# Performance work log

Hardware: AMD Instinct MI355X
Metric: run time of the kernel (lower is better)

The kernel has to match this reference:

```python
import jax, jax.numpy as jnp
import numpy as np

B, S, E, H = 2, 2048, 1024, 16
D = E // H


def setup_inputs() -> dict:
    key = jax.random.key(0)
    ks = jax.random.split(key, 7)
    return {
        "query": jax.random.normal(ks[0], (B, S, E), dtype=jnp.float32),
        "key": jax.random.normal(ks[1], (B, S, E), dtype=jnp.float32),
        "value": jax.random.normal(ks[2], (B, S, E), dtype=jnp.float32),
        "Wq": jax.random.normal(ks[3], (E, E), dtype=jnp.float32) * (E ** -0.5),
        "Wk": jax.random.normal(ks[4], (E, E), dtype=jnp.float32) * (E ** -0.5),
        "Wv": jax.random.normal(ks[5], (E, E), dtype=jnp.float32) * (E ** -0.5),
        "Wo": jax.random.normal(ks[6], (E, E), dtype=jnp.float32) * (E ** -0.5),
    }


def reference(query, key, value, Wq, Wk, Wv, Wo):
    emb_dim = query.shape[-1]
    h = H
    d = emb_dim // h
    # QuantLinear with all-None quantizers == plain Linear (no bias):
    # torch Linear computes x @ W.T with W of shape [out, in].
    q = query @ Wq.T   # [b, s, e]
    k = key @ Wk.T
    v = value @ Wv.T
    # b s (h d) -> b h s d
    def split_heads(x):
        b, s, e = x.shape
        return x.reshape(b, s, h, d).transpose(0, 2, 1, 3)
    q = split_heads(q)
    k = split_heads(k)
    v = split_heads(v)
    # NOTE: faithful to source — scale uses full emb_dim, not head_dim.
    scale = emb_dim ** (-0.5)
    scores = jnp.einsum('bhsd,bhtd->bhst', q * scale, k)  # [b,h,s,s]
    weights = jax.nn.softmax(scores, axis=-1)  # QuantIdentity(None) == identity; dropout p=0
    heads = jnp.einsum('bhst,bhtd->bhsd', weights, v)
    # b h s d -> b s (h d)
    b = heads.shape[0]
    out = heads.transpose(0, 2, 1, 3).reshape(b, -1, emb_dim)
    return out @ Wo.T
```

## Files before the change

kernel.cpp:

```cpp
#include <hip/hip_runtime.h>
#include <hip/hip_bf16.h>
#include <stdint.h>

typedef __attribute__((ext_vector_type(8))) short s16x8;
typedef __attribute__((ext_vector_type(4))) float f32x4;
typedef __attribute__((ext_vector_type(16))) float f32x16;

#define QSCALE 0.045084220027780106f

__device__ __forceinline__ unsigned short f2bf(float f) {
    union { float f; uint32_t u; } v; v.f = f;
    uint32_t u = v.u;
    u += 0x7FFFu + ((u >> 16) & 1u);
    return (unsigned short)(u >> 16);
}

__device__ __forceinline__ unsigned int pkbf2(float a, float b) {
    union { __hip_bfloat162 h; unsigned int u; } x;
    x.h = __float22bfloat162_rn(float2{a, b});
    return x.u;
}

#define GLOAD_LDS16(gptr, lptr)                                                         \
    __builtin_amdgcn_global_load_lds(                                                   \
        (const __attribute__((address_space(1))) unsigned int*)(gptr),                  \
        (__attribute__((address_space(3))) unsigned int*)(lptr), 16, 0, 0)

__global__ __launch_bounds__(256)
void cvt_all(const float* __restrict__ q, const float* __restrict__ k,
             const float* __restrict__ v, const float* __restrict__ wq,
             const float* __restrict__ wk, const float* __restrict__ wv,
             const float* __restrict__ wo,
             unsigned short* __restrict__ xq, unsigned short* __restrict__ xk,
             unsigned short* __restrict__ xv, unsigned short* __restrict__ wqb,
             unsigned short* __restrict__ wkb, unsigned short* __restrict__ wvb,
             unsigned short* __restrict__ wob)
{
    int bid = blockIdx.x;
    const float* src; unsigned short* dst; int rel;
    if (bid < 6144) {
        int s = bid >> 11; rel = bid & 2047;
        src = (s == 0) ? q : (s == 1) ? k : v;
        dst = (s == 0) ? xq : (s == 1) ? xk : xv;
    } else {
        int s = (bid - 6144) >> 9; rel = (bid - 6144) & 511;
        src = (s == 0) ? wq : (s == 1) ? wk : (s == 2) ? wv : wo;
        dst = (s == 0) ? wqb : (s == 1) ? wkb : (s == 2) ? wvb : wob;
    }
    size_t i = (size_t)rel * 256 + threadIdx.x;
    const float4* p = (const float4*)src;
    float4 a = p[i * 2];
    float4 b2 = p[i * 2 + 1];
    s16x8 r;
    r[0] = (short)f2bf(a.x);  r[1] = (short)f2bf(a.y);
    r[2] = (short)f2bf(a.z);  r[3] = (short)f2bf(a.w);
    r[4] = (short)f2bf(b2.x); r[5] = (short)f2bf(b2.y);
    r[6] = (short)f2bf(b2.z); r[7] = (short)f2bf(b2.w);
    *(s16x8*)(dst + i * 8) = r;
}

__device__ __forceinline__ void gemm_tile512(const unsigned short* __restrict__ A,
                                             const unsigned short* __restrict__ Bt,
                                             void* __restrict__ C,
                                             int N, int K, int f32out, float cscale,
                                             unsigned short* Al, unsigned short* Bl)
{
    const int tid  = threadIdx.x;
    const int lane = tid & 63;
    const int w    = tid >> 6;
    const int wr   = w >> 2, wc = w & 3;
    const int l15  = lane & 15, l4 = lane >> 4;

    const int m0 = blockIdx.x * 128;
    const int n0 = blockIdx.y * 128;

    f32x4 acc[4][2];
#pragma unroll
    for (int i = 0; i < 4; ++i)
#pragma unroll
        for (int j = 0; j < 2; ++j) acc[i][j] = (f32x4){0.f, 0.f, 0.f, 0.f};

    const int slin = w * 64 + lane;
    const int srow = slin >> 2;
    const int scol = ((slin & 3) ^ ((srow >> 1) & 3)) * 8;

    int aoff[4], boff[2];
#pragma unroll
    for (int mi = 0; mi < 4; ++mi) {
        int rowa = wr * 64 + mi * 16 + l15;
        aoff[mi] = rowa * 32 + ((l4 ^ ((rowa >> 1) & 3)) * 8);
    }
#pragma unroll
    for (int nf = 0; nf < 2; ++nf) {
        int rowb = wc * 32 + nf * 16 + l15;
        boff[nf] = rowb * 32 + ((l4 ^ ((rowb >> 1) & 3)) * 8);
    }

    for (int k0 = 0; k0 < K; k0 += 32) {
        {
            const unsigned short* gA = A + (size_t)(m0 + srow) * K + k0 + scol;
            GLOAD_LDS16(gA, Al + w * 512);
            const unsigned short* gB = Bt + (size_t)(n0 + srow) * K + k0 + scol;
            GLOAD_LDS16(gB, Bl + w * 512);
        }
        __syncthreads();
        s16x8 af[4], bfr[2];
#pragma unroll
        for (int mi = 0; mi < 4; ++mi) af[mi] = *(const s16x8*)(Al + aoff[mi]);
#pragma unroll
        for (int nf = 0; nf < 2; ++nf) bfr[nf] = *(const s16x8*)(Bl + boff[nf]);
#pragma unroll
        for (int mi = 0; mi < 4; ++mi)
#pragma unroll
            for (int nf = 0; nf < 2; ++nf)
                acc[mi][nf] = __builtin_amdgcn_mfma_f32_16x16x32_bf16(af[mi], bfr[nf], acc[mi][nf], 0, 0, 0);
        __syncthreads();
    }

#pragma unroll
    for (int mi = 0; mi < 4; ++mi)
#pragma unroll
        for (int nf = 0; nf < 2; ++nf)
#pragma unroll
            for (int r = 0; r < 4; ++r) {
                int row = m0 + wr * 64 + mi * 16 + l4 * 4 + r;
                int col = n0 + wc * 32 + nf * 16 + l15;
                float v = acc[mi][nf][r];
                if (f32out) ((float*)C)[(size_t)row * N + col] = v;
                else        ((unsigned short*)C)[(size_t)row * N + col] = f2bf(v * cscale);
            }
}

__global__ __launch_bounds__(512, 6)
void gemm_qkv(const unsigned short* __restrict__ A0, const unsigned short* __restrict__ A1,
              const unsigned short* __restrict__ A2,
              const unsigned short* __restrict__ B0, const unsigned short* __restrict__ B1,
              const unsigned short* __restrict__ B2,
              unsigned short* __restrict__ C0, unsigned short* __restrict__ C1,
              unsigned short* __restrict__ C2)
{
    __shared__ unsigned short Al[128 * 32];
    __shared__ unsigned short Bl[128 * 32];
    int z = blockIdx.z;
    const unsigned short* A  = (z == 0) ? A0 : (z == 1) ? A1 : A2;
    const unsigned short* Bt = (z == 0) ? B0 : (z == 1) ? B1 : B2;
    unsigned short*       C  = (z == 0) ? C0 : (z == 1) ? C1 : C2;
    float cscale = (z == 0) ? QSCALE : 1.0f;
    gemm_tile512(A, Bt, C, 1024, 1024, 0, cscale, Al, Bl);
}

__global__ __launch_bounds__(512, 6)
void gemm_out(const unsigned short* __restrict__ A, const unsigned short* __restrict__ Bt,
              float* __restrict__ C)
{
    __shared__ unsigned short Al[128 * 32];
    __shared__ unsigned short Bl[128 * 32];
    gemm_tile512(A, Bt, C, 1024, 1024, 1, 1.0f, Al, Bl);
}

__global__ __launch_bounds__(256)
void transpose_v(const unsigned short* __restrict__ Pv, unsigned short* __restrict__ Vt)
{
    __shared__ unsigned short T[64][72];
    const int t  = threadIdx.x;
    const int st = blockIdx.x, bh = blockIdx.y;
    const int b = bh >> 4, h = bh & 15;
    const int s0 = st * 64;
#pragma unroll
    for (int rp = 0; rp < 2; ++rp) {
        int sl = rp * 32 + (t >> 3);
        int dl = (t & 7) * 8;
        s16x8 v = *(const s16x8*)(Pv + (size_t)(b * 2048 + s0 + sl) * 1024 + h * 64 + dl);
        *(s16x8*)(&T[sl][dl]) = v;
    }
    __syncthreads();
#pragma unroll
    for (int rp = 0; rp < 2; ++rp) {
        int dl = rp * 32 + (t >> 3);
        int sl = (t & 7) * 8;
        s16x8 v;
#pragma unroll
        for (int j = 0; j < 8; ++j) v[j] = (short)T[sl + j][dl];
        *(s16x8*)(Vt + ((size_t)bh * 64 + dl) * 2048 + s0 + sl) = v;
    }
}

__global__ __launch_bounds__(512, 4)
void attn6(const unsigned short* __restrict__ Q,
           const unsigned short* __restrict__ Kp,
           const unsigned short* __restrict__ Vt,
           unsigned short* __restrict__ O)
{
    __shared__ unsigned short Kl[2][2][64 * 64];
    __shared__ unsigned short Vl[2][2][64 * 64];

    const int tid  = threadIdx.x;
    const int lane = tid & 63;
    const int w    = tid >> 6;
    const int half = w >> 2, ws = w & 3;
    const int q31  = lane & 31;
    const int lh   = lane >> 5;
    const int m7q  = q31 & 7;

    const int hw  = blockIdx.x;
    const int xcd = hw & 7;
    const int idx = hw >> 3;
    const int bh  = xcd * 4 + (idx >> 4);
    const int qt  = idx & 15;
    const int b = bh >> 4, hd = bh & 15;
    const int colbase = hd * 64;
    const int kvbase = half * 1024;

    const size_t qrow = (size_t)(b * 2048 + qt * 128 + ws * 32 + q31);
    s16x8 qf[4];
#pragma unroll
    for (int dk = 0; dk < 4; ++dk)
        qf[dk] = *(const s16x8*)(Q + qrow * 1024 + colbase + dk * 16 + lh * 8);

    int krow[2], kcol[2];
#pragma unroll
    for (int i = 0; i < 2; ++i) {
        int lin = (i * 4 + ws) * 64 + lane;
        krow[i] = lin >> 3;
        kcol[i] = ((lin & 7) ^ (krow[i] & 7)) * 8;
    }

    f32x16 oa[2] = {};
    float l_run = 0.f;

#define STAGE_KV(buf, kv0)                                                                     \
    {                                                                                          \
        _Pragma("unroll")                                                                      \
        for (int i = 0; i < 2; ++i) {                                                          \
            const unsigned short* gk = Kp + (size_t)(b * 2048 + (kv0) + krow[i]) * 1024        \
                                          + colbase + kcol[i];                                 \
            GLOAD_LDS16(gk, &Kl[half][buf][(i * 4 + ws) * 512]);                               \
            const unsigned short* gv = Vt + ((size_t)bh * 64 + krow[i]) * 2048                 \
                                          + (kv0) + kcol[i];                                   \
            GLOAD_LDS16(gv, &Vl[half][buf][(i * 4 + ws) * 512]);                               \
        }                                                                                      \
    }

    STAGE_KV(0, kvbase);
    __syncthreads();

    for (int kt = 0; kt < 16; ++kt) {
        const int cur = kt & 1;
        if (kt < 15) STAGE_KV(cur ^ 1, kvbase + (kt + 1) * 64);

        f32x16 s0 = {}, s1 = {};
#pragma unroll
        for (int dk = 0; dk < 4; ++dk) {
            const int sl = ((dk * 2 + lh) ^ m7q) * 8;
            s16x8 kf0 = *(const s16x8*)(&Kl[half][cur][q31 * 64 + sl]);
            s16x8 kf1 = *(const s16x8*)(&Kl[half][cur][(32 + q31) * 64 + sl]);
            s0 = __builtin_amdgcn_mfma_f32_32x32x16_bf16(kf0, qf[dk], s0, 0, 0, 0);
            s1 = __builtin_amdgcn_mfma_f32_32x32x16_bf16(kf1, qf[dk], s1, 0, 0, 0);
        }

        unsigned int PK[2][8];
        float ps = 0.f;
        {
            float p[16];
#pragma unroll
            for (int i = 0; i < 16; ++i) { p[i] = __builtin_amdgcn_exp2f(s0[i]); ps += p[i]; }
#pragma unroll
            for (int j = 0; j < 8; ++j) PK[0][j] = pkbf2(p[2 * j], p[2 * j + 1]);
#pragma unroll
            for (int i = 0; i < 16; ++i) { p[i] = __builtin_amdgcn_exp2f(s1[i]); ps += p[i]; }
#pragma unroll
            for (int j = 0; j < 8; ++j) PK[1][j] = pkbf2(p[2 * j], p[2 * j + 1]);
        }
        l_run += ps;

#pragma unroll
        for (int t = 0; t < 4; ++t) {
            const int bk = t >> 1, j0 = (t & 1) * 4;
            unsigned int A0 = PK[bk][j0],     C0 = PK[bk][j0 + 2];
            unsigned int A1 = PK[bk][j0 + 1], C1 = PK[bk][j0 + 3];
            unsigned int sA0 = (unsigned int)__shfl_xor((int)A0, 32, 64);
            unsigned int sC0 = (unsigned int)__shfl_xor((int)C0, 32, 64);
            unsigned int sA1 = (unsigned int)__shfl_xor((int)A1, 32, 64);
            unsigned int sC1 = (unsigned int)__shfl_xor((int)C1, 32, 64);
            union { unsigned int u[4]; s16x8 v; } pa;
            pa.u[0] = lh ? sC0 : A0;
            pa.u[1] = lh ? sC1 : A1;
            pa.u[2] = lh ? C0 : sA0;
            pa.u[3] = lh ? C1 : sA1;
            const int slv = ((t * 2 + lh) ^ m7q) * 8;
            s16x8 vf0 = *(const s16x8*)(&Vl[half][cur][q31 * 64 + slv]);
            s16x8 vf1 = *(const s16x8*)(&Vl[half][cur][(32 + q31) * 64 + slv]);
            oa[0] = __builtin_amdgcn_mfma_f32_32x32x16_bf16(vf0, pa.v, oa[0], 0, 0, 0);
            oa[1] = __builtin_amdgcn_mfma_f32_32x32x16_bf16(vf1, pa.v, oa[1], 0, 0, 0);
        }
        __syncthreads();
    }

    l_run += __shfl_xor(l_run, 32, 64);

    f32x4* Xch = (f32x4*)&Kl[0][0][0];
    float*  Lx = (float*)&Vl[0][0][0];

    if (half == 1) {
#pragma unroll
        for (int dh = 0; dh < 2; ++dh)
#pragma unroll
            for (int rg = 0; rg < 4; ++rg) {
                f32x4 c = { oa[dh][rg * 4 + 0], oa[dh][rg * 4 + 1],
                            oa[dh][rg * 4 + 2], oa[dh][rg * 4 + 3] };
                Xch[((ws * 8 + dh * 4 + rg) << 6) + lane] = c;
            }
        if (lh == 0) Lx[ws * 32 + q31] = l_run;
    }
    __syncthreads();
    if (half == 0) {
        const float lt  = l_run + Lx[ws * 32 + q31];
        const float inv = 1.0f / lt;
#pragma unroll
        for (int dh = 0; dh < 2; ++dh)
#pragma unroll
            for (int rg = 0; rg < 4; ++rg) {
                f32x4 po = Xch[((ws * 8 + dh * 4 + rg) << 6) + lane];
                const int d0 = dh * 32 + rg * 8 + lh * 4;
                uint2 pw;
                pw.x = pkbf2((oa[dh][rg * 4 + 0] + po[0]) * inv,
                             (oa[dh][rg * 4 + 1] + po[1]) * inv);
                pw.y = pkbf2((oa[dh][rg * 4 + 2] + po[2]) * inv,
                             (oa[dh][rg * 4 + 3] + po[3]) * inv);
                *(uint2*)(O + qrow * 1024 + colbase + d0) = pw;
            }
    }
#undef STAGE_KV
}

extern "C" void kernel_launch(void* const* d_in, const int* in_sizes, int n_in,
                              void* d_out, int out_size, void* d_ws, size_t ws_size,
                              hipStream_t stream)
{
    const float* query = (const float*)d_in[0];
    const float* key   = (const float*)d_in[1];
    const float* value = (const float*)d_in[2];
    const float* Wq    = (const float*)d_in[3];
    const float* Wk    = (const float*)d_in[4];
    const float* Wv    = (const float*)d_in[5];
    const float* Wo    = (const float*)d_in[6];
    float* out = (float*)d_out;

    char* ws = (char*)d_ws;
    const size_t SZX = (size_t)4096 * 1024 * 2;
    const size_t SZW = (size_t)1024 * 1024 * 2;
    unsigned short* Xq  = (unsigned short*)(ws + 0);
    unsigned short* Xk  = (unsigned short*)(ws + SZX);
    unsigned short* Xv  = (unsigned short*)(ws + 2 * SZX);
    unsigned short* Wqb = (unsigned short*)(ws + 3 * SZX);
    unsigned short* Wkb = (unsigned short*)(ws + 3 * SZX + SZW);
    unsigned short* Wvb = (unsigned short*)(ws + 3 * SZX + 2 * SZW);
    unsigned short* Wob = (unsigned short*)(ws + 3 * SZX + 3 * SZW);
    unsigned short* Pq  = (unsigned short*)(ws + 3 * SZX + 4 * SZW);
    unsigned short* Pk  = (unsigned short*)(ws + 4 * SZX + 4 * SZW);
    unsigned short* Pv  = (unsigned short*)(ws + 5 * SZX + 4 * SZW);
    unsigned short* AO  = (unsigned short*)(ws + 6 * SZX + 4 * SZW);
    unsigned short* Vt  = Xq;

    cvt_all<<<8192, 256, 0, stream>>>(query, key, value, Wq, Wk, Wv, Wo,
                                      Xq, Xk, Xv, Wqb, Wkb, Wvb, Wob);
    gemm_qkv<<<dim3(32, 8, 3), 512, 0, stream>>>(Xq, Xk, Xv, Wqb, Wkb, Wvb, Pq, Pk, Pv);
    transpose_v<<<dim3(32, 32), 256, 0, stream>>>(Pv, Vt);
    attn6<<<512, 512, 0, stream>>>(Pq, Pk, Vt, AO);
    gemm_out<<<dim3(32, 8), 512, 0, stream>>>(AO, Wob, out);
}
```

Before: 129.0 us.

## Fuse V transpose into QKV GEMM epilogue and software-pipeline PV in attention

The V projection GEMM now writes its output already transposed to head-major Vt through a shared-memory staging tile, so the separate transpose kernel and its extra round trip through global memory go away. The attention kernel now loads K for the next tile one step ahead and loads V for the current tile. It defers the P·V MFMA of the previous tile so that it overlaps with the QK MFMAs and exp of the current tile. This costs extra registers for the saved P fragments and extra LDS and barriers in the GEMM epilogue.

New measurement: 126.6 us. About the same (-1.8%).

```diff
diff --git a/kernel.cpp b/kernel.cpp
--- a/kernel.cpp
+++ b/kernel.cpp
@@ -62,8 +62,9 @@
 __device__ __forceinline__ void gemm_tile512(const unsigned short* __restrict__ A,
                                              const unsigned short* __restrict__ Bt,
                                              void* __restrict__ C,
-                                             int N, int K, int f32out, float cscale,
-                                             unsigned short* Al, unsigned short* Bl)
+                                             int N, int K, int mode, float cscale,
+                                             unsigned short* Al, unsigned short* Bl,
+                                             unsigned short* Tl)
 {
     const int tid  = threadIdx.x;
     const int lane = tid & 63;
@@ -117,6 +118,38 @@
         __syncthreads();
     }
 
+    if (mode == 2) {
+        const int b_  = m0 >> 11;
+        const int s0g = m0 & 2047;
+#pragma unroll
+        for (int c0 = 0; c0 < 128; c0 += 32) {
+            if (wc == (c0 >> 5)) {
+#pragma unroll
+                for (int mi = 0; mi < 4; ++mi)
+#pragma unroll
+                    for (int nf = 0; nf < 2; ++nf) {
+                        uint2 pw;
+                        pw.x = pkbf2(acc[mi][nf][0], acc[mi][nf][1]);
+                        pw.y = pkbf2(acc[mi][nf][2], acc[mi][nf][3]);
+                        int c  = nf * 16 + l15;
+                        int s4 = wr * 64 + mi * 16 + l4 * 4;
+                        *(uint2*)&Tl[c * 136 + s4] = pw;
+                    }
+            }
+            __syncthreads();
+            {
+                int d  = tid >> 4;
+                int sg = tid & 15;
+                s16x8 v = *(const s16x8*)&Tl[d * 136 + sg * 8];
+                int colg  = n0 + c0 + d;
+                int vtrow = (b_ * 16 + (colg >> 6)) * 64 + (colg & 63);
+                *(s16x8*)((unsigned short*)C + (size_t)vtrow * 2048 + s0g + sg * 8) = v;
+            }
+            __syncthreads();
+        }
+        return;
+    }
+
 #pragma unroll
     for (int mi = 0; mi < 4; ++mi)
 #pragma unroll
@@ -126,8 +159,8 @@
                 int row = m0 + wr * 64 + mi * 16 + l4 * 4 + r;
                 int col = n0 + wc * 32 + nf * 16 + l15;
                 float v = acc[mi][nf][r];
-                if (f32out) ((float*)C)[(size_t)row * N + col] = v;
-                else        ((unsigned short*)C)[(size_t)row * N + col] = f2bf(v * cscale);
+                if (mode == 1) ((float*)C)[(size_t)row * N + col] = v;
+                else           ((unsigned short*)C)[(size_t)row * N + col] = f2bf(v * cscale);
             }
 }
 
@@ -141,12 +174,14 @@
 {
     __shared__ unsigned short Al[128 * 32];
     __shared__ unsigned short Bl[128 * 32];
+    __shared__ unsigned short Tl[32 * 136];
     int z = blockIdx.z;
     const unsigned short* A  = (z == 0) ? A0 : (z == 1) ? A1 : A2;
     const unsigned short* Bt = (z == 0) ? B0 : (z == 1) ? B1 : B2;
     unsigned short*       C  = (z == 0) ? C0 : (z == 1) ? C1 : C2;
     float cscale = (z == 0) ? QSCALE : 1.0f;
-    gemm_tile512(A, Bt, C, 1024, 1024, 0, cscale, Al, Bl);
+    int mode = (z == 2) ? 2 : 0;
+    gemm_tile512(A, Bt, C, 1024, 1024, mode, cscale, Al, Bl, Tl);
 }
 
 __global__ __launch_bounds__(512, 6)
@@ -155,38 +190,11 @@
 {
     __shared__ unsigned short Al[128 * 32];
     __shared__ unsigned short Bl[128 * 32];
-    gemm_tile512(A, Bt, C, 1024, 1024, 1, 1.0f, Al, Bl);
-}
-
-__global__ __launch_bounds__(256)
-void transpose_v(const unsigned short* __restrict__ Pv, unsigned short* __restrict__ Vt)
-{
-    __shared__ unsigned short T[64][72];
-    const int t  = threadIdx.x;
-    const int st = blockIdx.x, bh = blockIdx.y;
-    const int b = bh >> 4, h = bh & 15;
-    const int s0 = st * 64;
-#pragma unroll
-    for (int rp = 0; rp < 2; ++rp) {
-        int sl = rp * 32 + (t >> 3);
-        int dl = (t & 7) * 8;
-        s16x8 v = *(const s16x8*)(Pv + (size_t)(b * 2048 + s0 + sl) * 1024 + h * 64 + dl);
-        *(s16x8*)(&T[sl][dl]) = v;
-    }
-    __syncthreads();
-#pragma unroll
-    for (int rp = 0; rp < 2; ++rp) {
-        int dl = rp * 32 + (t >> 3);
-        int sl = (t & 7) * 8;
-        s16x8 v;
-#pragma unroll
-        for (int j = 0; j < 8; ++j) v[j] = (short)T[sl + j][dl];
-        *(s16x8*)(Vt + ((size_t)bh * 64 + dl) * 2048 + s0 + sl) = v;
-    }
+    gemm_tile512(A, Bt, C, 1024, 1024, 1, 1.0f, Al, Bl, nullptr);
 }
 
 __global__ __launch_bounds__(512, 4)
-void attn6(const unsigned short* __restrict__ Q,
+void attn7(const unsigned short* __restrict__ Q,
            const unsigned short* __restrict__ Kp,
            const unsigned short* __restrict__ Vt,
            unsigned short* __restrict__ O)
@@ -228,25 +236,57 @@
     f32x16 oa[2] = {};
     float l_run = 0.f;
 
-#define STAGE_KV(buf, kv0)                                                                     \
+#define STAGE_K(buf, kv0)                                                                      \
     {                                                                                          \
         _Pragma("unroll")                                                                      \
         for (int i = 0; i < 2; ++i) {                                                          \
             const unsigned short* gk = Kp + (size_t)(b * 2048 + (kv0) + krow[i]) * 1024        \
                                           + colbase + kcol[i];                                 \
             GLOAD_LDS16(gk, &Kl[half][buf][(i * 4 + ws) * 512]);                               \
+        }                                                                                      \
+    }
+#define STAGE_V(buf, kv0)                                                                      \
+    {                                                                                          \
+        _Pragma("unroll")                                                                      \
+        for (int i = 0; i < 2; ++i) {                                                          \
             const unsigned short* gv = Vt + ((size_t)bh * 64 + krow[i]) * 2048                 \
                                           + (kv0) + kcol[i];                                   \
             GLOAD_LDS16(gv, &Vl[half][buf][(i * 4 + ws) * 512]);                               \
         }                                                                                      \
     }
-
-    STAGE_KV(0, kvbase);
+#define PV_STEP(vb)                                                                            \
+    {                                                                                          \
+        _Pragma("unroll")                                                                      \
+        for (int t = 0; t < 4; ++t) {                                                          \
+            const int bk = t >> 1, j0 = (t & 1) * 4;                                           \
+            unsigned int A0 = PKp[bk][j0],     C0 = PKp[bk][j0 + 2];                           \
+            unsigned int A1 = PKp[bk][j0 + 1], C1 = PKp[bk][j0 + 3];                           \
+            unsigned int sA0 = (unsigned int)__shfl_xor((int)A0, 32, 64);                      \
+            unsigned int sC0 = (unsigned int)__shfl_xor((int)C0, 32, 64);                      \
+            unsigned int sA1 = (unsigned int)__shfl_xor((int)A1, 32, 64);                      \
+            unsigned int sC1 = (unsigned int)__shfl_xor((int)C1, 32, 64);                      \
+            union { unsigned int u[4]; s16x8 v; } pa;                                          \
+            pa.u[0] = lh ? sC0 : A0;                                                           \
+            pa.u[1] = lh ? sC1 : A1;                                                           \
+            pa.u[2] = lh ? C0 : sA0;                                                           \
+            pa.u[3] = lh ? C1 : sA1;                                                           \
+            const int slv = ((t * 2 + lh) ^ m7q) * 8;                                          \
+            s16x8 vf0 = *(const s16x8*)(&Vl[half][vb][q31 * 64 + slv]);                        \
+            s16x8 vf1 = *(const s16x8*)(&Vl[half][vb][(32 + q31) * 64 + slv]);                 \
+            oa[0] = __builtin_amdgcn_mfma_f32_32x32x16_bf16(vf0, pa.v, oa[0], 0, 0, 0);        \
+            oa[1] = __builtin_amdgcn_mfma_f32_32x32x16_bf16(vf1, pa.v, oa[1], 0, 0, 0);        \
+        }                                                                                      \
+    }
+
+    unsigned int PKp[2][8];
+
+    STAGE_K(0, kvbase);
     __syncthreads();
 
     for (int kt = 0; kt < 16; ++kt) {
         const int cur = kt & 1;
-        if (kt < 15) STAGE_KV(cur ^ 1, kvbase + (kt + 1) * 64);
+        if (kt < 15) STAGE_K(cur ^ 1, kvbase + (kt + 1) * 64);
+        STAGE_V(cur, kvbase + kt * 64);
 
         f32x16 s0 = {}, s1 = {};
 #pragma unroll
@@ -258,43 +298,32 @@
             s1 = __builtin_amdgcn_mfma_f32_32x32x16_bf16(kf1, qf[dk], s1, 0, 0, 0);
         }
 
-        unsigned int PK[2][8];
+        if (kt > 0) PV_STEP(cur ^ 1);
+
+        unsigned int PKc[2][8];
         float ps = 0.f;
         {
             float p[16];
 #pragma unroll
             for (int i = 0; i < 16; ++i) { p[i] = __builtin_amdgcn_exp2f(s0[i]); ps += p[i]; }
 #pragma unroll
-            for (int j = 0; j < 8; ++j) PK[0][j] = pkbf2(p[2 * j], p[2 * j + 1]);
+            for (int j = 0; j < 8; ++j) PKc[0][j] = pkbf2(p[2 * j], p[2 * j + 1]);
 #pragma unroll
             for (int i = 0; i < 16; ++i) { p[i] = __builtin_amdgcn_exp2f(s1[i]); ps += p[i]; }
 #pragma unroll
-            for (int j = 0; j < 8; ++j) PK[1][j] = pkbf2(p[2 * j], p[2 * j + 1]);
+            for (int j = 0; j < 8; ++j) PKc[1][j] = pkbf2(p[2 * j], p[2 * j + 1]);
         }
         l_run += ps;
 
 #pragma unroll
-        for (int t = 0; t < 4; ++t) {
-            const int bk = t >> 1, j0 = (t & 1) * 4;
-            unsigned int A0 = PK[bk][j0],     C0 = PK[bk][j0 + 2];
-            unsigned int A1 = PK[bk][j0 + 1], C1 = PK[bk][j0 + 3];
-            unsigned int sA0 = (unsigned int)__shfl_xor((int)A0, 32, 64);
-            unsigned int sC0 = (unsigned int)__shfl_xor((int)C0, 32, 64);
-            unsigned int sA1 = (unsigned int)__shfl_xor((int)A1, 32, 64);
-            unsigned int sC1 = (unsigned int)__shfl_xor((int)C1, 32, 64);
-            union { unsigned int u[4]; s16x8 v; } pa;
-            pa.u[0] = lh ? sC0 : A0;
-            pa.u[1] = lh ? sC1 : A1;
-            pa.u[2] = lh ? C0 : sA0;
-            pa.u[3] = lh ? C1 : sA1;
-            const int slv = ((t * 2 + lh) ^ m7q) * 8;
-            s16x8 vf0 = *(const s16x8*)(&Vl[half][cur][q31 * 64 + slv]);
-            s16x8 vf1 = *(const s16x8*)(&Vl[half][cur][(32 + q31) * 64 + slv]);
-            oa[0] = __builtin_amdgcn_mfma_f32_32x32x16_bf16(vf0, pa.v, oa[0], 0, 0, 0);
-            oa[1] = __builtin_amdgcn_mfma_f32_32x32x16_bf16(vf1, pa.v, oa[1], 0, 0, 0);
-        }
+        for (int bk = 0; bk < 2; ++bk)
+#pragma unroll
+            for (int j = 0; j < 8; ++j) PKp[bk][j] = PKc[bk][j];
+
         __syncthreads();
     }
+
+    PV_STEP(1);
 
     l_run += __shfl_xor(l_run, 32, 64);
 
@@ -330,7 +359,9 @@
                 *(uint2*)(O + qrow * 1024 + colbase + d0) = pw;
             }
     }
-#undef STAGE_KV
+#undef STAGE_K
+#undef STAGE_V
+#undef PV_STEP
 }
 
 extern "C" void kernel_launch(void* const* d_in, const int* in_sizes, int n_in,
@@ -358,14 +389,12 @@
     unsigned short* Wob = (unsigned short*)(ws + 3 * SZX + 3 * SZW);
     unsigned short* Pq  = (unsigned short*)(ws + 3 * SZX + 4 * SZW);
     unsigned short* Pk  = (unsigned short*)(ws + 4 * SZX + 4 * SZW);
-    unsigned short* Pv  = (unsigned short*)(ws + 5 * SZX + 4 * SZW);
+    unsigned short* Vt  = (unsigned short*)(ws + 5 * SZX + 4 * SZW);
     unsigned short* AO  = (unsigned short*)(ws + 6 * SZX + 4 * SZW);
-    unsigned short* Vt  = Xq;
 
     cvt_all<<<8192, 256, 0, stream>>>(query, key, value, Wq, Wk, Wv, Wo,
                                       Xq, Xk, Xv, Wqb, Wkb, Wvb, Wob);
-    gemm_qkv<<<dim3(32, 8, 3), 512, 0, stream>>>(Xq, Xk, Xv, Wqb, Wkb, Wvb, Pq, Pk, Pv);
-    transpose_v<<<dim3(32, 32), 256, 0, stream>>>(Pv, Vt);
-    attn6<<<512, 512, 0, stream>>>(Pq, Pk, Vt, AO);
+    gemm_qkv<<<dim3(32, 8, 3), 512, 0, stream>>>(Xq, Xk, Xv, Wqb, Wkb, Wvb, Pq, Pk, Vt);
+    attn7<<<512, 512, 0, stream>>>(Pq, Pk, Vt, AO);
     gemm_out<<<dim3(32, 8), 512, 0, stream>>>(AO, Wob, out);
 }
```

## Fuse V transpose into QKV GEMM epilogue and refine LDS swizzle in attention

Applied to the files above, without the earlier changes.

The V projection GEMM now writes its output directly in the transposed per-head layout that attention needs. It stages each tile through a shared-memory buffer, which removes the separate transpose kernel launch and one full round-trip of V through global memory. Separately, the attention kernel's K/V shared-memory XOR swizzle gains an extra term based on the row group, aimed at reducing LDS bank conflicts. The fused epilogue adds shared memory and barriers to every QKV block, which can lower occupancy or slow the GEMM tail.

New measurement: 123.7 us. 4.0% less time.

```diff
diff --git a/kernel.cpp b/kernel.cpp
--- a/kernel.cpp
+++ b/kernel.cpp
@@ -62,8 +62,9 @@
 __device__ __forceinline__ void gemm_tile512(const unsigned short* __restrict__ A,
                                              const unsigned short* __restrict__ Bt,
                                              void* __restrict__ C,
-                                             int N, int K, int f32out, float cscale,
-                                             unsigned short* Al, unsigned short* Bl)
+                                             int N, int K, int mode, float cscale,
+                                             unsigned short* Al, unsigned short* Bl,
+                                             unsigned short* Tl)
 {
     const int tid  = threadIdx.x;
     const int lane = tid & 63;
@@ -117,6 +118,38 @@
         __syncthreads();
     }
 
+    if (mode == 2) {
+        const int b_  = m0 >> 11;
+        const int s0g = m0 & 2047;
+#pragma unroll
+        for (int c0 = 0; c0 < 128; c0 += 32) {
+            if (wc == (c0 >> 5)) {
+#pragma unroll
+                for (int mi = 0; mi < 4; ++mi)
+#pragma unroll
+                    for (int nf = 0; nf < 2; ++nf) {
+                        uint2 pw;
+                        pw.x = pkbf2(acc[mi][nf][0], acc[mi][nf][1]);
+                        pw.y = pkbf2(acc[mi][nf][2], acc[mi][nf][3]);
+                        int c  = nf * 16 + l15;
+                        int s4 = wr * 64 + mi * 16 + l4 * 4;
+                        *(uint2*)&Tl[c * 136 + s4] = pw;
+                    }
+            }
+            __syncthreads();
+            {
+                int d  = tid >> 4;
+                int sg = tid & 15;
+                s16x8 v = *(const s16x8*)&Tl[d * 136 + sg * 8];
+                int colg  = n0 + c0 + d;
+                int vtrow = (b_ * 16 + (colg >> 6)) * 64 + (colg & 63);
+                *(s16x8*)((unsigned short*)C + (size_t)vtrow * 2048 + s0g + sg * 8) = v;
+            }
+            __syncthreads();
+        }
+        return;
+    }
+
 #pragma unroll
     for (int mi = 0; mi < 4; ++mi)
 #pragma unroll
@@ -126,8 +159,8 @@
                 int row = m0 + wr * 64 + mi * 16 + l4 * 4 + r;
                 int col = n0 + wc * 32 + nf * 16 + l15;
                 float v = acc[mi][nf][r];
-                if (f32out) ((float*)C)[(size_t)row * N + col] = v;
-                else        ((unsigned short*)C)[(size_t)row * N + col] = f2bf(v * cscale);
+                if (mode == 1) ((float*)C)[(size_t)row * N + col] = v;
+                else           ((unsigned short*)C)[(size_t)row * N + col] = f2bf(v * cscale);
             }
 }
 
@@ -141,12 +174,14 @@
 {
     __shared__ unsigned short Al[128 * 32];
     __shared__ unsigned short Bl[128 * 32];
+    __shared__ unsigned short Tl[32 * 136];
     int z = blockIdx.z;
     const unsigned short* A  = (z == 0) ? A0 : (z == 1) ? A1 : A2;
     const unsigned short* Bt = (z == 0) ? B0 : (z == 1) ? B1 : B2;
     unsigned short*       C  = (z == 0) ? C0 : (z == 1) ? C1 : C2;
     float cscale = (z == 0) ? QSCALE : 1.0f;
-    gemm_tile512(A, Bt, C, 1024, 1024, 0, cscale, Al, Bl);
+    int mode = (z == 2) ? 2 : 0;
+    gemm_tile512(A, Bt, C, 1024, 1024, mode, cscale, Al, Bl, Tl);
 }
 
 __global__ __launch_bounds__(512, 6)
@@ -155,38 +190,11 @@
 {
     __shared__ unsigned short Al[128 * 32];
     __shared__ unsigned short Bl[128 * 32];
-    gemm_tile512(A, Bt, C, 1024, 1024, 1, 1.0f, Al, Bl);
-}
-
-__global__ __launch_bounds__(256)
-void transpose_v(const unsigned short* __restrict__ Pv, unsigned short* __restrict__ Vt)
-{
-    __shared__ unsigned short T[64][72];
-    const int t  = threadIdx.x;
-    const int st = blockIdx.x, bh = blockIdx.y;
-    const int b = bh >> 4, h = bh & 15;
-    const int s0 = st * 64;
-#pragma unroll
-    for (int rp = 0; rp < 2; ++rp) {
-        int sl = rp * 32 + (t >> 3);
-        int dl = (t & 7) * 8;
-        s16x8 v = *(const s16x8*)(Pv + (size_t)(b * 2048 + s0 + sl) * 1024 + h * 64 + dl);
-        *(s16x8*)(&T[sl][dl]) = v;
-    }
-    __syncthreads();
-#pragma unroll
-    for (int rp = 0; rp < 2; ++rp) {
-        int dl = rp * 32 + (t >> 3);
-        int sl = (t & 7) * 8;
-        s16x8 v;
-#pragma unroll
-        for (int j = 0; j < 8; ++j) v[j] = (short)T[sl + j][dl];
-        *(s16x8*)(Vt + ((size_t)bh * 64 + dl) * 2048 + s0 + sl) = v;
-    }
+    gemm_tile512(A, Bt, C, 1024, 1024, 1, 1.0f, Al, Bl, nullptr);
 }
 
 __global__ __launch_bounds__(512, 4)
-void attn6(const unsigned short* __restrict__ Q,
+void attn8(const unsigned short* __restrict__ Q,
            const unsigned short* __restrict__ Kp,
            const unsigned short* __restrict__ Vt,
            unsigned short* __restrict__ O)
@@ -201,6 +209,7 @@
     const int q31  = lane & 31;
     const int lh   = lane >> 5;
     const int m7q  = q31 & 7;
+    const int j2   = ((q31 >> 3) & 3) << 1;
 
     const int hw  = blockIdx.x;
     const int xcd = hw & 7;
@@ -222,7 +231,8 @@
     for (int i = 0; i < 2; ++i) {
         int lin = (i * 4 + ws) * 64 + lane;
         krow[i] = lin >> 3;
-        kcol[i] = ((lin & 7) ^ (krow[i] & 7)) * 8;
+        int u   = lin & 7;
+        kcol[i] = ((u ^ (krow[i] & 7) ^ (((krow[i] >> 3) & 3) << 1)) * 8);
     }
 
     f32x16 oa[2] = {};
@@ -251,7 +261,7 @@
         f32x16 s0 = {}, s1 = {};
 #pragma unroll
         for (int dk = 0; dk < 4; ++dk) {
-            const int sl = ((dk * 2 + lh) ^ m7q) * 8;
+            const int sl = (((dk * 2 + lh) ^ m7q ^ j2) * 8);
             s16x8 kf0 = *(const s16x8*)(&Kl[half][cur][q31 * 64 + sl]);
             s16x8 kf1 = *(const s16x8*)(&Kl[half][cur][(32 + q31) * 64 + sl]);
             s0 = __builtin_amdgcn_mfma_f32_32x32x16_bf16(kf0, qf[dk], s0, 0, 0, 0);
@@ -287,7 +297,7 @@
             pa.u[1] = lh ? sC1 : A1;
             pa.u[2] = lh ? C0 : sA0;
             pa.u[3] = lh ? C1 : sA1;
-            const int slv = ((t * 2 + lh) ^ m7q) * 8;
+            const int slv = (((t * 2 + lh) ^ m7q ^ j2) * 8);
             s16x8 vf0 = *(const s16x8*)(&Vl[half][cur][q31 * 64 + slv]);
             s16x8 vf1 = *(const s16x8*)(&Vl[half][cur][(32 + q31) * 64 + slv]);
             oa[0] = __builtin_amdgcn_mfma_f32_32x32x16_bf16(vf0, pa.v, oa[0], 0, 0, 0);
@@ -358,14 +368,12 @@
     unsigned short* Wob = (unsigned short*)(ws + 3 * SZX + 3 * SZW);
     unsigned short* Pq  = (unsigned short*)(ws + 3 * SZX + 4 * SZW);
     unsigned short* Pk  = (unsigned short*)(ws + 4 * SZX + 4 * SZW);
-    unsigned short* Pv  = (unsigned short*)(ws + 5 * SZX + 4 * SZW);
+    unsigned short* Vt  = (unsigned short*)(ws + 5 * SZX + 4 * SZW);
     unsigned short* AO  = (unsigned short*)(ws + 6 * SZX + 4 * SZW);
-    unsigned short* Vt  = Xq;
 
     cvt_all<<<8192, 256, 0, stream>>>(query, key, value, Wq, Wk, Wv, Wo,
                                       Xq, Xk, Xv, Wqb, Wkb, Wvb, Wob);
-    gemm_qkv<<<dim3(32, 8, 3), 512, 0, stream>>>(Xq, Xk, Xv, Wqb, Wkb, Wvb, Pq, Pk, Pv);
-    transpose_v<<<dim3(32, 32), 256, 0, stream>>>(Pv, Vt);
-    attn6<<<512, 512, 0, stream>>>(Pq, Pk, Vt, AO);
+    gemm_qkv<<<dim3(32, 8, 3), 512, 0, stream>>>(Xq, Xk, Xv, Wqb, Wkb, Wvb, Pq, Pk, Vt);
+    attn8<<<512, 512, 0, stream>>>(Pq, Pk, Vt, AO);
     gemm_out<<<dim3(32, 8), 512, 0, stream>>>(AO, Wob, out);
 }
```
